# Performance work log

Measured on AMD Instinct MI355X. Metric: run time of the kernel, lower is better.

## Reference

```python
import jax, jax.numpy as jnp
from jax import lax
import numpy as np

B, TIN, F, H, TOUT = 256, 512, 64, 512, 64


def setup_inputs() -> dict:
    key = jax.random.key(0)
    ks = jax.random.split(key, 16)
    s = 0.05

    def p(k, shape):
        return jax.random.normal(k, shape, jnp.float32) * s

    inp = {
        "x": jax.random.normal(ks[0], (B, TIN, F), jnp.float32),
        "y": jax.random.normal(ks[1], (B, TOUT), jnp.float32),
    }
    i = 2
    for name, insz in [("enc0", F), ("enc1", H), ("dec0", 1), ("dec1", H)]:
        inp[name + "_Wih"] = p(ks[i], (4 * H, insz)); i += 1
        inp[name + "_Whh"] = p(ks[i], (4 * H, H)); i += 1
        inp[name + "_bih"] = jnp.zeros((4 * H,), jnp.float32)
        inp[name + "_bhh"] = jnp.zeros((4 * H,), jnp.float32)
    inp["proj_W"] = p(ks[i], (1, H)); i += 1
    inp["proj_b"] = jnp.zeros((1,), jnp.float32)
    return inp


def _cell(xt, h, c, Wih, Whh, bih, bhh):
    # PyTorch gate order: i, f, g, o
    g = xt @ Wih.T + h @ Whh.T + bih + bhh  # [B, 4H]
    i, f, gg, o = jnp.split(g, 4, axis=-1)
    c = jax.nn.sigmoid(f) * c + jax.nn.sigmoid(i) * jnp.tanh(gg)
    h = jax.nn.sigmoid(o) * jnp.tanh(c)
    return h, c


def reference(x, y,
              enc0_Wih, enc0_Whh, enc0_bih, enc0_bhh,
              enc1_Wih, enc1_Whh, enc1_bih, enc1_bhh,
              dec0_Wih, dec0_Whh, dec0_bih, dec0_bhh,
              dec1_Wih, dec1_Whh, dec1_bih, dec1_bhh,
              proj_W, proj_b):
    Bsz = x.shape[0]
    Hd = enc0_Whh.shape[1]
    Tout = y.shape[1]
    z = jnp.zeros((Bsz, Hd), x.dtype)

    def enc_step(carry, xt):
        h0, c0, h1, c1 = carry
        h0, c0 = _cell(xt, h0, c0, enc0_Wih, enc0_Whh, enc0_bih, enc0_bhh)
        h1, c1 = _cell(h0, h1, c1, enc1_Wih, enc1_Whh, enc1_bih, enc1_bhh)
        return (h0, c0, h1, c1), None

    (h0, c0, h1, c1), _ = lax.scan(enc_step, (z, z, z, z), jnp.swapaxes(x, 0, 1))

    prev = x[:, -1, -1:]  # [B, 1]

    def dec_step(carry, _):
        h0, c0, h1, c1, prev = carry
        h0, c0 = _cell(prev, h0, c0, dec0_Wih, dec0_Whh, dec0_bih, dec0_bhh)
        h1, c1 = _cell(h0, h1, c1, dec1_Wih, dec1_Whh, dec1_bih, dec1_bhh)
        step = h1 @ proj_W.T + proj_b  # [B, 1]
        # teacher_forcing = 0.0 -> always feed model prediction back
        return (h0, c0, h1, c1, step), step[:, 0]

    _, outs = lax.scan(dec_step, (h0, c0, h1, c1, prev), None, length=Tout)
    return outs.T  # [B, Tout]
```

## Files before the change

### kernel.cpp

```cpp
#include <hip/hip_runtime.h>

#define TINN 512
#define FF 64
#define HHD 512
#define TOUTN 64

using v8h = __attribute__((ext_vector_type(8))) _Float16;
using v4h = __attribute__((ext_vector_type(4))) _Float16;
using v4f = __attribute__((ext_vector_type(4))) float;
using u32x4 = __attribute__((ext_vector_type(4))) unsigned int;
using u64 = unsigned long long;

#define AGT __HIP_MEMORY_SCOPE_AGENT

#define WOFF 0
#define BIAS_OFF 131072
#define WIH0_OFF 131328
#define PREV_OFF 131584
#define PART_OFF 131840
#define PROJW_OFF 132864
#define PROJB_OFF 134912
#define TRANS_OFF 134976
#define SMEM_TOTAL 137024

#define WS_BAR 0
#define WS_HOFF 16384
#define HBYTES (256 * HHD * 2)
#define WS_XS (WS_HOFF + 6 * HBYTES)
#define XS_TBYTES 32768
#define WS_NEED (WS_XS + (size_t)TINN * XS_TBYTES)

static __device__ __forceinline__ float sigm(float x) { return 1.0f / (1.0f + __expf(-x)); }
static __device__ __forceinline__ float tanh_f(float x) { return 1.0f - 2.0f / (1.0f + __expf(2.0f * x)); }

static __device__ __forceinline__ v8h aload16(const _Float16* p) {
  union { u64 u[2]; v8h h; } c;
  const u64* q = (const u64*)p;
  c.u[0] = __hip_atomic_load(q, __ATOMIC_RELAXED, AGT);
  c.u[1] = __hip_atomic_load(q + 1, __ATOMIC_RELAXED, AGT);
  return c.h;
}
static __device__ __forceinline__ void astore8(_Float16* p, v4h v) {
  union { u64 u; v4h h; } c;
  c.h = v;
  __hip_atomic_store((u64*)p, c.u, __ATOMIC_RELAXED, AGT);
}
static __device__ __forceinline__ void astore8z(void* p) {
  __hip_atomic_store((u64*)p, 0ull, __ATOMIC_RELAXED, AGT);
}

#if __has_builtin(__builtin_amdgcn_raw_ptr_buffer_load_b128) && \
    __has_builtin(__builtin_amdgcn_make_buffer_rsrc)
#define HAVE_BUFLOAD 1
using rsrc_t = __amdgpu_buffer_rsrc_t;
static __device__ __forceinline__ rsrc_t mkrsrc(const void* p) {
  return __builtin_amdgcn_make_buffer_rsrc((void*)p, (short)0, 0xFFFFFFFFu, 0x00020000);
}
static __device__ __forceinline__ v8h bload16(rsrc_t r, int byteOff) {
  union { u32x4 u; v8h h; } c;
  c.u = __builtin_amdgcn_raw_ptr_buffer_load_b128(r, byteOff, 0, 17);
  return c.h;
}
#endif

static __device__ __forceinline__ void signalDone(unsigned* slots, int mySlot, unsigned val) {
  __builtin_amdgcn_s_waitcnt(0);
  __syncthreads();
  if (threadIdx.x == 0)
    __hip_atomic_store(&slots[(size_t)mySlot * 16], val, __ATOMIC_RELAXED, AGT);
}

static __device__ __forceinline__ void waitRole(unsigned* slots, int base, int tgt) {
  if (tgt > 0) {
    if (threadIdx.x < 32) {
      while ((int)__hip_atomic_load(&slots[(size_t)(base + threadIdx.x) * 16],
                                    __ATOMIC_RELAXED, AGT) < tgt)
        __builtin_amdgcn_s_sleep(1);
    }
    __syncthreads();
#if __has_builtin(__builtin_amdgcn_sched_barrier)
    __builtin_amdgcn_sched_barrier(0);
#endif
  }
}

static __device__ __forceinline__ void waitRoles(unsigned* slots, int tgt0, int tgt1) {
  int t = threadIdx.x;
  if (t < 64) {
    int tgt = (t < 32) ? tgt0 : tgt1;
    if (tgt > 0) {
      unsigned* p = &slots[(size_t)t * 16];
      while ((int)__hip_atomic_load(p, __ATOMIC_RELAXED, AGT) < tgt)
        __builtin_amdgcn_s_sleep(1);
    }
  }
  __syncthreads();
#if __has_builtin(__builtin_amdgcn_sched_barrier)
  __builtin_amdgcn_sched_barrier(0);
#endif
}

static __device__ __attribute__((noinline)) void loadWeights(
    int tid, int hc0, const float* W1, int ld1, int K1,
    const float* W2, int K) {
  extern __shared__ char smem[];
  int c = tid >> 2, sub = tid & 3;
  int nt = c >> 4, l = c & 15;
  int n = nt * HHD + hc0 + l;
  int Kq = K >> 2;
  for (int k = sub * Kq; k < (sub + 1) * Kq; ++k) {
    float v;
    if (k < K1) v = W1[(size_t)n * ld1 + k];
    else        v = W2[(size_t)n * HHD + (k - K1)];
    int kc = k >> 6, ks = (k >> 5) & 1, quad = (k >> 3) & 3, j = k & 7;
    int off = (((kc * 2 + ks) * 4 + nt) * 64 + quad * 16 + l) * 16 + j * 2;
    *(_Float16*)(smem + WOFF + off) = (_Float16)v;
  }
}

template <int WC0>
static __device__ __forceinline__ void mfma8(
    const _Float16* src, int rt, int lane, const char* wbLane, v4f* acc) {
#if HAVE_BUFLOAD
  rsrc_t rs = mkrsrc(src);
#endif
#pragma unroll
  for (int kc = 0; kc < 8; ++kc) {
    int off = rt * 16384 + kc * 2048 + lane * 16;
    v8h ak0, ak1;
#if HAVE_BUFLOAD
    ak0 = bload16(rs, off);
    ak1 = bload16(rs, off + 1024);
#else
    ak0 = aload16(src + off / 2);
    ak1 = aload16(src + (off + 1024) / 2);
#endif
    const char* bb = wbLane + (size_t)(WC0 + kc) * 8192;
#pragma unroll
    for (int ks = 0; ks < 2; ++ks) {
      v8h a = ks ? ak1 : ak0;
      acc[0] = __builtin_amdgcn_mfma_f32_16x16x32_f16(a, *(const v8h*)(bb + (ks * 4 + 0) * 1024), acc[0], 0, 0, 0);
      acc[1] = __builtin_amdgcn_mfma_f32_16x16x32_f16(a, *(const v8h*)(bb + (ks * 4 + 1) * 1024), acc[1], 0, 0, 0);
      acc[2] = __builtin_amdgcn_mfma_f32_16x16x32_f16(a, *(const v8h*)(bb + (ks * 4 + 2) * 1024), acc[2], 0, 0, 0);
      acc[3] = __builtin_amdgcn_mfma_f32_16x16x32_f16(a, *(const v8h*)(bb + (ks * 4 + 3) * 1024), acc[3], 0, 0, 0);
    }
  }
}

static __device__ __forceinline__ void mfmaDual(
    const _Float16* h0src, const _Float16* h1src, int rt, int lane,
    const char* wbLane, v4f* acc) {
  v8h a1[16], a0[16];
#if HAVE_BUFLOAD
  rsrc_t r1 = mkrsrc(h1src);
  rsrc_t r0 = mkrsrc(h0src);
#pragma unroll
  for (int kc = 0; kc < 8; ++kc) {
    int off = rt * 16384 + kc * 2048 + lane * 16;
    a1[2 * kc]     = bload16(r1, off);
    a1[2 * kc + 1] = bload16(r1, off + 1024);
  }
#pragma unroll
  for (int kc = 0; kc < 8; ++kc) {
    int off = rt * 16384 + kc * 2048 + lane * 16;
    a0[2 * kc]     = bload16(r0, off);
    a0[2 * kc + 1] = bload16(r0, off + 1024);
  }
#else
#pragma unroll
  for (int kc = 0; kc < 8; ++kc) {
    int off = rt * 16384 + kc * 2048 + lane * 16;
    a1[2 * kc]     = aload16(h1src + off / 2);
    a1[2 * kc + 1] = aload16(h1src + (off + 1024) / 2);
  }
#pragma unroll
  for (int kc = 0; kc < 8; ++kc) {
    int off = rt * 16384 + kc * 2048 + lane * 16;
    a0[2 * kc]     = aload16(h0src + off / 2);
    a0[2 * kc + 1] = aload16(h0src + (off + 1024) / 2);
  }
#endif
#pragma unroll
  for (int kc = 0; kc < 8; ++kc) {
    const char* bb = wbLane + (size_t)(8 + kc) * 8192;
#pragma unroll
    for (int ks = 0; ks < 2; ++ks) {
      v8h a = a1[2 * kc + ks];
      acc[0] = __builtin_amdgcn_mfma_f32_16x16x32_f16(a, *(const v8h*)(bb + (ks * 4 + 0) * 1024), acc[0], 0, 0, 0);
      acc[1] = __builtin_amdgcn_mfma_f32_16x16x32_f16(a, *(const v8h*)(bb + (ks * 4 + 1) * 1024), acc[1], 0, 0, 0);
      acc[2] = __builtin_amdgcn_mfma_f32_16x16x32_f16(a, *(const v8h*)(bb + (ks * 4 + 2) * 1024), acc[2], 0, 0, 0);
      acc[3] = __builtin_amdgcn_mfma_f32_16x16x32_f16(a, *(const v8h*)(bb + (ks * 4 + 3) * 1024), acc[3], 0, 0, 0);
    }
  }
#pragma unroll
  for (int kc = 0; kc < 8; ++kc) {
    const char* bb = wbLane + (size_t)kc * 8192;
#pragma unroll
    for (int ks = 0; ks < 2; ++ks) {
      v8h a = a0[2 * kc + ks];
      acc[0] = __builtin_amdgcn_mfma_f32_16x16x32_f16(a, *(const v8h*)(bb + (ks * 4 + 0) * 1024), acc[0], 0, 0, 0);
      acc[1] = __builtin_amdgcn_mfma_f32_16x16x32_f16(a, *(const v8h*)(bb + (ks * 4 + 1) * 1024), acc[1], 0, 0, 0);
      acc[2] = __builtin_amdgcn_mfma_f32_16x16x32_f16(a, *(const v8h*)(bb + (ks * 4 + 2) * 1024), acc[2], 0, 0, 0);
      acc[3] = __builtin_amdgcn_mfma_f32_16x16x32_f16(a, *(const v8h*)(bb + (ks * 4 + 3) * 1024), acc[3], 0, 0, 0);
    }
  }
}

static __device__ __forceinline__ void xChunk(
    const char* xsT, const float* xstep, int m0, int tid,
    const char* wbLane, v4f* acc) {
  int lane = tid & 63, wave = tid >> 6;
  int l15 = lane & 15, quad = lane >> 4;
  v8h ak0, ak1;
  if (xsT != nullptr) {
    int rt = (m0 >> 4) + wave;
    const char* xb = xsT + rt * 2048 + lane * 16;
    ak0 = *(const v8h*)(xb);
    ak1 = *(const v8h*)(xb + 1024);
  } else {
    int ra = m0 + wave * 16 + l15;
    const float* xr = xstep + (size_t)ra * (TINN * FF) + quad * 8;
    v4f f00 = *(const v4f*)(xr);
    v4f f01 = *(const v4f*)(xr + 4);
    v4f f10 = *(const v4f*)(xr + 32);
    v4f f11 = *(const v4f*)(xr + 36);
#pragma unroll
    for (int e = 0; e < 4; ++e) {
      ak0[e] = (_Float16)f00[e]; ak0[4 + e] = (_Float16)f01[e];
      ak1[e] = (_Float16)f10[e]; ak1[4 + e] = (_Float16)f11[e];
    }
  }
#pragma unroll
  for (int ks = 0; ks < 2; ++ks) {
    v8h a = ks ? ak1 : ak0;
    acc[0] = __builtin_amdgcn_mfma_f32_16x16x32_f16(a, *(const v8h*)(wbLane + (ks * 4 + 0) * 1024), acc[0], 0, 0, 0);
    acc[1] = __builtin_amdgcn_mfma_f32_16x16x32_f16(a, *(const v8h*)(wbLane + (ks * 4 + 1) * 1024), acc[1], 0, 0, 0);
    acc[2] = __builtin_amdgcn_mfma_f32_16x16x32_f16(a, *(const v8h*)(wbLane + (ks * 4 + 2) * 1024), acc[2], 0, 0, 0);
    acc[3] = __builtin_amdgcn_mfma_f32_16x16x32_f16(a, *(const v8h*)(wbLane + (ks * 4 + 3) * 1024), acc[3], 0, 0, 0);
  }
}

static __device__ __forceinline__ void epilogue(
    int tid, int m0, int hc0, int rank1, _Float16* hout, float* creg, v4f* acc) {
  extern __shared__ char smem[];
  int lane = tid & 63, wave = tid >> 6;
  int l15 = lane & 15, quad = lane >> 4;
  float* bias = (float*)(smem + BIAS_OFF);
  float bi = bias[l15], bf = bias[16 + l15], bg = bias[32 + l15], bo = bias[48 + l15];
  float wi = 0.f, wf = 0.f, wg = 0.f, wo = 0.f;
  if (rank1) {
    float* wih0 = (float*)(smem + WIH0_OFF);
    wi = wih0[l15]; wf = wih0[16 + l15]; wg = wih0[32 + l15]; wo = wih0[48 + l15];
  }
  float* prevl = (float*)(smem + PREV_OFF);
  _Float16* tb = (_Float16*)(smem + TRANS_OFF + (size_t)wave * 512);
#pragma unroll
  for (int r = 0; r < 4; ++r) {
    int mloc = wave * 16 + quad * 4 + r;
    float gi = acc[0][r] + bi, gf = acc[1][r] + bf;
    float gg = acc[2][r] + bg, go = acc[3][r] + bo;
    if (rank1) {
      float pv = prevl[mloc];
      gi += pv * wi; gf += pv * wf; gg += pv * wg; go += pv * wo;
    }
    float cc = sigm(gf) * creg[r] + sigm(gi) * tanh_f(gg);
    float h = sigm(go) * tanh_f(cc);
    creg[r] = cc;
    tb[(quad * 4 + r) * 16 + l15] = (_Float16)h;
  }
  {
    int mloc = lane & 15, cg = lane >> 4;
    v4h hv = *(const v4h*)(tb + mloc * 16 + cg * 4);
    int m = m0 + wave * 16 + mloc;
    int c0 = hc0 + cg * 4;
    int off = (m >> 4) * 16384 + (c0 >> 6) * 2048 + ((c0 >> 5) & 1) * 1024 +
              ((c0 >> 3) & 3) * 256 + (m & 15) * 16 + (c0 & 7) * 2;
    astore8((_Float16*)((char*)hout + off), hv);
  }
}


static __device__ __attribute__((noinline)) void stepEnc0(
    int tid, int m0, int hc0, unsigned* slots, int mySlot, int p,
    const char* xsT, const float* xstep,
    const _Float16* h0prev, _Float16* h0out, float* creg) {
  extern __shared__ char smem[];
  int lane = tid & 63, wave = tid >> 6;
  v4f acc[4];
  acc[0] = v4f{0.f, 0.f, 0.f, 0.f}; acc[1] = acc[0]; acc[2] = acc[0]; acc[3] = acc[0];
  const char* wbLane = smem + WOFF + (size_t)lane * 16;
  if (p == 0) {
    waitRoles(slots, 1, 0);
    xChunk(xsT, xstep, m0, tid, wbLane, acc);
  } else {
    xChunk(xsT, xstep, m0, tid, wbLane, acc);
    waitRoles(slots, p + 1, p - 2);
  }
  mfma8<1>(h0prev, (m0 >> 4) + wave, lane, wbLane, acc);
  epilogue(tid, m0, hc0, 0, h0out, creg, acc);
  signalDone(slots, mySlot, p + 2);
}

static __device__ __attribute__((noinline)) void stepL1(
    int tid, int m0, int hc0, unsigned* slots, int mySlot, int tR1, int tR0,
    const _Float16* h0src, const _Float16* h1prev, _Float16* h1out, float* creg) {
  extern __shared__ char smem[];
  int lane = tid & 63, wave = tid >> 6;
  v4f acc[4];
  acc[0] = v4f{0.f, 0.f, 0.f, 0.f}; acc[1] = acc[0]; acc[2] = acc[0]; acc[3] = acc[0];
  const char* wbLane = smem + WOFF + (size_t)lane * 16;
  int rt = (m0 >> 4) + wave;
  waitRoles(slots, tR0, tR1);
  mfmaDual(h0src, h1prev, rt, lane, wbLane, acc);
  epilogue(tid, m0, hc0, 0, h1out, creg, acc);
  signalDone(slots, mySlot, tR0);
}

static __device__ __attribute__((noinline)) void stepDec0(
    int tid, int m0, int hc0, unsigned* slots, int mySlot, int u,
    const _Float16* h0prev, _Float16* h0out, float* creg) {
  extern __shared__ char smem[];
  int lane = tid & 63, wave = tid >> 6;
  v4f acc[4];
  acc[0] = v4f{0.f, 0.f, 0.f, 0.f}; acc[1] = acc[0]; acc[2] = acc[0]; acc[3] = acc[0];
  const char* wbLane = smem + WOFF + (size_t)lane * 16;
  waitRole(slots, 0, u + 1);
  mfma8<0>(h0prev, (m0 >> 4) + wave, lane, wbLane, acc);
  epilogue(tid, m0, hc0, 1, h0out, creg, acc);
  signalDone(slots, mySlot, u + 2);
}

__global__ void __launch_bounds__(256, 1)
seq2seq_kernel(const float* x,
               const float* e0wi, const float* e0wh, const float* e0bi, const float* e0bh,
               const float* e1wi, const float* e1wh, const float* e1bi, const float* e1bh,
               const float* d0wi, const float* d0wh, const float* d0bi, const float* d0bh,
               const float* d1wi, const float* d1wh, const float* d1bi, const float* d1bh,
               const float* pw, const float* pb,
               float* out, char* ws, int useXs) {
  extern __shared__ char smem[];
  int tid = threadIdx.x, bid = blockIdx.x;
  int group = bid >> 6;
  int r = bid & 63;
  bool isL1 = (r >= 32);
  int hcTile = r & 31;
  int hc0 = hcTile * 16;
  int m0 = group * 64;
  unsigned* slots = (unsigned*)(ws + WS_BAR) + (size_t)group * 1024;
  int mySlot = isL1 ? 32 + hcTile : hcTile;
  char* xs = useXs ? (ws + WS_XS) : nullptr;

  _Float16* h0b[4]; _Float16* h1b[2];
  h0b[0] = (_Float16*)(ws + WS_HOFF);
  h0b[1] = (_Float16*)(ws + WS_HOFF + 1 * HBYTES);
  h0b[2] = (_Float16*)(ws + WS_HOFF + 2 * HBYTES);
  h0b[3] = (_Float16*)(ws + WS_HOFF + 3 * HBYTES);
  h1b[0] = (_Float16*)(ws + WS_HOFF + 4 * HBYTES);
  h1b[1] = (_Float16*)(ws + WS_HOFF + 5 * HBYTES);

  float creg[4];
  creg[0] = 0.f; creg[1] = 0.f; creg[2] = 0.f; creg[3] = 0.f;

  {
    int t16 = r * 256 + tid;
    char* base = (t16 < 8192) ? (char*)h0b[3] : (char*)h1b[1];
    int idx = t16 & 8191;
    astore8z(base + (size_t)m0 * HHD * 2 + (size_t)idx * 8);
  }

  if (xs) {
    int m = m0 + (tid & 63);
    int cb = (tid >> 6) * 16;
    int rt = m >> 4, l15m = m & 15;
    for (int k = 0; k < 8; ++k) {
      int t = r + k * 64;
      const float* xp = x + (size_t)m * (TINN * FF) + (size_t)t * FF + cb;
      v4f f0 = *(const v4f*)(xp);
      v4f f1 = *(const v4f*)(xp + 4);
      v4f f2 = *(const v4f*)(xp + 8);
      v4f f3 = *(const v4f*)(xp + 12);
      v4h h0_, h1_, h2_, h3_;
#pragma unroll
      for (int e = 0; e < 4; ++e) {
        h0_[e] = (_Float16)f0[e]; h1_[e] = (_Float16)f1[e];
        h2_[e] = (_Float16)f2[e]; h3_[e] = (_Float16)f3[e];
      }
      char* xt = xs + (size_t)t * XS_TBYTES;
      v4h hs[4] = {h0_, h1_, h2_, h3_};
#pragma unroll
      for (int s = 0; s < 4; ++s) {
        int c0 = cb + 4 * s;
        int off = (rt * 2 + ((c0 >> 5) & 1)) * 1024 +
                  ((c0 >> 3) & 3) * 256 + l15m * 16 + (c0 & 7) * 2;
        astore8((_Float16*)(xt + off), hs[s]);
      }
    }
  }

  if (!isL1) {
    loadWeights(tid, hc0, e0wi, 64, 64, e0wh, 576);
    if (tid < 64) {
      int n = (tid >> 4) * HHD + hc0 + (tid & 15);
      ((float*)(smem + BIAS_OFF))[tid] = e0bi[n] + e0bh[n];
    }
  } else {
    loadWeights(tid, hc0, e1wi, 512, 512, e1wh, 1024);
    if (tid < 64) {
      int n = (tid >> 4) * HHD + hc0 + (tid & 15);
      ((float*)(smem + BIAS_OFF))[tid] = e1bi[n] + e1bh[n];
    }
  }
  signalDone(slots, mySlot, 1);

  if (!isL1) {
    for (int p = 0; p < TINN; ++p)
      stepEnc0(tid, m0, hc0, slots, mySlot, p,
               xs ? xs + (size_t)p * XS_TBYTES : nullptr,
               xs ? nullptr : x + (size_t)p * FF,
               h0b[(p + 3) & 3], h0b[p & 3], creg);
    loadWeights(tid, hc0, d0wh, 512, 512, nullptr, 512);
    if (tid < 64) {
      int n = (tid >> 4) * HHD + hc0 + (tid & 15);
      ((float*)(smem + BIAS_OFF))[tid] = d0bi[n] + d0bh[n];
      ((float*)(smem + WIH0_OFF))[tid] = d0wi[n];
    }
    for (int k = tid; k < 512; k += 256) ((float*)(smem + PROJW_OFF))[k] = pw[k];
    if (tid == 0) ((float*)(smem + PROJB_OFF))[0] = pb[0];
    for (int t = 0; t <= TOUTN; ++t) {
      int u = TINN + t;
      waitRole(slots, 32, u + 1);
      float* prevl = (float*)(smem + PREV_OFF);
      if (t == 0) {
        if (tid < 64)
          prevl[tid] = x[(size_t)(m0 + tid) * (TINN * FF) + 511 * 64 + 63];
      } else {
        float* part = (float*)(smem + PART_OFF);
        float* pjw = (float*)(smem + PROJW_OFF);
        const _Float16* h1base = h1b[(u + 1) & 1];
        int m = m0 + (tid >> 2);
        int rt = m >> 4, l15m = m & 15;
        int kc0 = (tid & 3) * 2;
        float s = 0.f;
#pragma unroll
        for (int kc = kc0; kc < kc0 + 2; ++kc)
#pragma unroll
          for (int ks = 0; ks < 2; ++ks)
#pragma unroll
            for (int q = 0; q < 4; ++q) {
              int off = (rt * 8 + kc) * 2048 + ks * 1024 + q * 256 + l15m * 16;
              v8h hv = aload16(h1base + off / 2);
              const float* w = pjw + kc * 64 + ks * 32 + q * 8;
#pragma unroll
              for (int e = 0; e < 8; ++e) s += (float)hv[e] * w[e];
            }
        part[tid] = s;
        __syncthreads();
        if (tid < 64) {
          float p4 = part[tid * 4] + part[tid * 4 + 1] + part[tid * 4 + 2] +
                     part[tid * 4 + 3] + ((float*)(smem + PROJB_OFF))[0];
          prevl[tid] = p4;
          if (hcTile == 0) out[(size_t)(m0 + tid) * TOUTN + (t - 1)] = p4;
        }
      }
      __syncthreads();
      if (t < TOUTN)
        stepDec0(tid, m0, hc0, slots, mySlot, u, h0b[(u + 3) & 3], h0b[u & 3], creg);
    }
  } else {
    for (int s = 0; s < TINN; ++s)
      stepL1(tid, m0, hc0, slots, mySlot, s + 1, s + 2,
             h0b[s & 3], h1b[(s + 1) & 1], h1b[s & 1], creg);
    loadWeights(tid, hc0, d1wi, 512, 512, d1wh, 1024);
    if (tid < 64) {
      int n = (tid >> 4) * HHD + hc0 + (tid & 15);
      ((float*)(smem + BIAS_OFF))[tid] = d1bi[n] + d1bh[n];
    }
    for (int t = 0; t < TOUTN; ++t) {
      int u = TINN + t;
      stepL1(tid, m0, hc0, slots, mySlot, u + 1, u + 2,
             h0b[u & 3], h1b[(u + 1) & 1], h1b[u & 1], creg);
    }
  }
}

extern "C" void kernel_launch(void* const* d_in, const int* in_sizes, int n_in,
                              void* d_out, int out_size, void* d_ws, size_t ws_size,
                              hipStream_t stream) {
  const float* x = (const float*)d_in[0];
  const float* e0wi = (const float*)d_in[2];
  const float* e0wh = (const float*)d_in[3];
  const float* e0bi = (const float*)d_in[4];
  const float* e0bh = (const float*)d_in[5];
  const float* e1wi = (const float*)d_in[6];
  const float* e1wh = (const float*)d_in[7];
  const float* e1bi = (const float*)d_in[8];
  const float* e1bh = (const float*)d_in[9];
  const float* d0wi = (const float*)d_in[10];
  const float* d0wh = (const float*)d_in[11];
  const float* d0bi = (const float*)d_in[12];
  const float* d0bh = (const float*)d_in[13];
  const float* d1wi = (const float*)d_in[14];
  const float* d1wh = (const float*)d_in[15];
  const float* d1bi = (const float*)d_in[16];
  const float* d1bh = (const float*)d_in[17];
  const float* pw = (const float*)d_in[18];
  const float* pb = (const float*)d_in[19];

  int useXs = (ws_size >= WS_NEED) ? 1 : 0;
  (void)hipFuncSetAttribute((const void*)seq2seq_kernel,
                            hipFuncAttributeMaxDynamicSharedMemorySize, SMEM_TOTAL);
  (void)hipMemsetAsync(d_ws, 0, 16384, stream);
  seq2seq_kernel<<<dim3(256), dim3(256), SMEM_TOTAL, stream>>>(
      x, e0wi, e0wh, e0bi, e0bh, e1wi, e1wh, e1bi, e1bh,
      d0wi, d0wh, d0bi, d0bh, d1wi, d1wh, d1bi, d1bh,
      pw, pb, (float*)d_out, (char*)d_ws, useXs);
}
```

Before: 4.478 ms.

## Replicate completion flags per consumer block to avoid shared-slot polling contention

```diff
diff --git a/kernel.cpp b/kernel.cpp
--- a/kernel.cpp
+++ b/kernel.cpp
@@ -24,7 +24,8 @@
 #define SMEM_TOTAL 137024
 
 #define WS_BAR 0
-#define WS_HOFF 16384
+#define WS_FLAG_BYTES (4 * 64 * 64 * 64)
+#define WS_HOFF WS_FLAG_BYTES
 #define HBYTES (256 * HHD * 2)
 #define WS_XS (WS_HOFF + 6 * HBYTES)
 #define XS_TBYTES 32768
@@ -63,18 +64,20 @@
 }
 #endif
 
-static __device__ __forceinline__ void signalDone(unsigned* slots, int mySlot, unsigned val) {
+static __device__ __forceinline__ void signalDone(unsigned* flagsG, int mySlot, unsigned val) {
   __builtin_amdgcn_s_waitcnt(0);
   __syncthreads();
-  if (threadIdx.x == 0)
-    __hip_atomic_store(&slots[(size_t)mySlot * 16], val, __ATOMIC_RELAXED, AGT);
-}
-
-static __device__ __forceinline__ void waitRole(unsigned* slots, int base, int tgt) {
+  if (threadIdx.x < 64) {
+    unsigned* p = flagsG + ((size_t)threadIdx.x * 64 + mySlot) * 16;
+    __hip_atomic_store(p, val, __ATOMIC_RELAXED, AGT);
+  }
+}
+
+static __device__ __forceinline__ void waitRolePriv(unsigned* myflags, int base, int tgt) {
   if (tgt > 0) {
     if (threadIdx.x < 32) {
-      while ((int)__hip_atomic_load(&slots[(size_t)(base + threadIdx.x) * 16],
-                                    __ATOMIC_RELAXED, AGT) < tgt)
+      unsigned* p = myflags + (size_t)(base + threadIdx.x) * 16;
+      while ((int)__hip_atomic_load(p, __ATOMIC_RELAXED, AGT) < tgt)
         __builtin_amdgcn_s_sleep(1);
     }
     __syncthreads();
@@ -84,12 +87,12 @@
   }
 }
 
-static __device__ __forceinline__ void waitRoles(unsigned* slots, int tgt0, int tgt1) {
+static __device__ __forceinline__ void waitRolesPriv(unsigned* myflags, int tgt0, int tgt1) {
   int t = threadIdx.x;
   if (t < 64) {
     int tgt = (t < 32) ? tgt0 : tgt1;
     if (tgt > 0) {
-      unsigned* p = &slots[(size_t)t * 16];
+      unsigned* p = myflags + (size_t)t * 16;
       while ((int)__hip_atomic_load(p, __ATOMIC_RELAXED, AGT) < tgt)
         __builtin_amdgcn_s_sleep(1);
     }
@@ -281,7 +284,7 @@
 
 
 static __device__ __attribute__((noinline)) void stepEnc0(
-    int tid, int m0, int hc0, unsigned* slots, int mySlot, int p,
+    int tid, int m0, int hc0, unsigned* flagsG, unsigned* myflags, int mySlot, int p,
     const char* xsT, const float* xstep,
     const _Float16* h0prev, _Float16* h0out, float* creg) {
   extern __shared__ char smem[];
@@ -290,19 +293,20 @@
   acc[0] = v4f{0.f, 0.f, 0.f, 0.f}; acc[1] = acc[0]; acc[2] = acc[0]; acc[3] = acc[0];
   const char* wbLane = smem + WOFF + (size_t)lane * 16;
   if (p == 0) {
-    waitRoles(slots, 1, 0);
+    waitRolesPriv(myflags, 1, 0);
     xChunk(xsT, xstep, m0, tid, wbLane, acc);
   } else {
     xChunk(xsT, xstep, m0, tid, wbLane, acc);
-    waitRoles(slots, p + 1, p - 2);
+    waitRolesPriv(myflags, p + 1, p - 2);
   }
   mfma8<1>(h0prev, (m0 >> 4) + wave, lane, wbLane, acc);
   epilogue(tid, m0, hc0, 0, h0out, creg, acc);
-  signalDone(slots, mySlot, p + 2);
+  signalDone(flagsG, mySlot, p + 2);
 }
 
 static __device__ __attribute__((noinline)) void stepL1(
-    int tid, int m0, int hc0, unsigned* slots, int mySlot, int tR1, int tR0,
+    int tid, int m0, int hc0, unsigned* flagsG, unsigned* myflags, int mySlot,
+    int tR1, int tR0,
     const _Float16* h0src, const _Float16* h1prev, _Float16* h1out, float* creg) {
   extern __shared__ char smem[];
   int lane = tid & 63, wave = tid >> 6;
@@ -310,24 +314,24 @@
   acc[0] = v4f{0.f, 0.f, 0.f, 0.f}; acc[1] = acc[0]; acc[2] = acc[0]; acc[3] = acc[0];
   const char* wbLane = smem + WOFF + (size_t)lane * 16;
   int rt = (m0 >> 4) + wave;
-  waitRoles(slots, tR0, tR1);
+  waitRolesPriv(myflags, tR0, tR1);
   mfmaDual(h0src, h1prev, rt, lane, wbLane, acc);
   epilogue(tid, m0, hc0, 0, h1out, creg, acc);
-  signalDone(slots, mySlot, tR0);
+  signalDone(flagsG, mySlot, tR0);
 }
 
 static __device__ __attribute__((noinline)) void stepDec0(
-    int tid, int m0, int hc0, unsigned* slots, int mySlot, int u,
+    int tid, int m0, int hc0, unsigned* flagsG, unsigned* myflags, int mySlot, int u,
     const _Float16* h0prev, _Float16* h0out, float* creg) {
   extern __shared__ char smem[];
   int lane = tid & 63, wave = tid >> 6;
   v4f acc[4];
   acc[0] = v4f{0.f, 0.f, 0.f, 0.f}; acc[1] = acc[0]; acc[2] = acc[0]; acc[3] = acc[0];
   const char* wbLane = smem + WOFF + (size_t)lane * 16;
-  waitRole(slots, 0, u + 1);
+  waitRolePriv(myflags, 0, u + 1);
   mfma8<0>(h0prev, (m0 >> 4) + wave, lane, wbLane, acc);
   epilogue(tid, m0, hc0, 1, h0out, creg, acc);
-  signalDone(slots, mySlot, u + 2);
+  signalDone(flagsG, mySlot, u + 2);
 }
 
 __global__ void __launch_bounds__(256, 1)
@@ -346,7 +350,8 @@
   int hcTile = r & 31;
   int hc0 = hcTile * 16;
   int m0 = group * 64;
-  unsigned* slots = (unsigned*)(ws + WS_BAR) + (size_t)group * 1024;
+  unsigned* flagsG = (unsigned*)(ws + WS_BAR) + (size_t)group * 64 * 64 * 16;
+  unsigned* myflags = flagsG + (size_t)r * 64 * 16;
   int mySlot = isL1 ? 32 + hcTile : hcTile;
   char* xs = useXs ? (ws + WS_XS) : nullptr;
 
@@ -410,11 +415,11 @@
       ((float*)(smem + BIAS_OFF))[tid] = e1bi[n] + e1bh[n];
     }
   }
-  signalDone(slots, mySlot, 1);
+  signalDone(flagsG, mySlot, 1);
 
   if (!isL1) {
     for (int p = 0; p < TINN; ++p)
-      stepEnc0(tid, m0, hc0, slots, mySlot, p,
+      stepEnc0(tid, m0, hc0, flagsG, myflags, mySlot, p,
                xs ? xs + (size_t)p * XS_TBYTES : nullptr,
                xs ? nullptr : x + (size_t)p * FF,
                h0b[(p + 3) & 3], h0b[p & 3], creg);
@@ -428,7 +433,7 @@
     if (tid == 0) ((float*)(smem + PROJB_OFF))[0] = pb[0];
     for (int t = 0; t <= TOUTN; ++t) {
       int u = TINN + t;
-      waitRole(slots, 32, u + 1);
+      waitRolePriv(myflags, 32, u + 1);
       float* prevl = (float*)(smem + PREV_OFF);
       if (t == 0) {
         if (tid < 64)
@@ -464,11 +469,12 @@
       }
       __syncthreads();
       if (t < TOUTN)
-        stepDec0(tid, m0, hc0, slots, mySlot, u, h0b[(u + 3) & 3], h0b[u & 3], creg);
+        stepDec0(tid, m0, hc0, flagsG, myflags, mySlot, u,
+                 h0b[(u + 3) & 3], h0b[u & 3], creg);
     }
   } else {
     for (int s = 0; s < TINN; ++s)
-      stepL1(tid, m0, hc0, slots, mySlot, s + 1, s + 2,
+      stepL1(tid, m0, hc0, flagsG, myflags, mySlot, s + 1, s + 2,
              h0b[s & 3], h1b[(s + 1) & 1], h1b[s & 1], creg);
     loadWeights(tid, hc0, d1wi, 512, 512, d1wh, 1024);
     if (tid < 64) {
@@ -477,7 +483,7 @@
     }
     for (int t = 0; t < TOUTN; ++t) {
       int u = TINN + t;
-      stepL1(tid, m0, hc0, slots, mySlot, u + 1, u + 2,
+      stepL1(tid, m0, hc0, flagsG, myflags, mySlot, u + 1, u + 2,
              h0b[u & 3], h1b[(u + 1) & 1], h1b[u & 1], creg);
     }
   }
@@ -509,7 +515,7 @@
   int useXs = (ws_size >= WS_NEED) ? 1 : 0;
   (void)hipFuncSetAttribute((const void*)seq2seq_kernel,
                             hipFuncAttributeMaxDynamicSharedMemorySize, SMEM_TOTAL);
-  (void)hipMemsetAsync(d_ws, 0, 16384, stream);
+  (void)hipMemsetAsync(d_ws, 0, WS_FLAG_BYTES, stream);
   seq2seq_kernel<<<dim3(256), dim3(256), SMEM_TOTAL, stream>>>(
       x, e0wi, e0wh, e0bi, e0bh, e1wi, e1wh, e1bi, e1bh,
       d0wi, d0wh, d0bi, d0bh, d1wi, d1wh, d1bi, d1bh,
```

After: 4.453 ms. About the same (-0.5%).

## Replace per-block flag slots with shared atomic counters and drop x pre-staging

Applied to the files above, without the earlier changes.

```diff
diff --git a/kernel.cpp b/kernel.cpp
--- a/kernel.cpp
+++ b/kernel.cpp
@@ -23,15 +23,18 @@
 #define TRANS_OFF 134976
 #define SMEM_TOTAL 137024
 
-#define WS_BAR 0
+#define WS_CNT 0
 #define WS_HOFF 16384
 #define HBYTES (256 * HHD * 2)
-#define WS_XS (WS_HOFF + 6 * HBYTES)
-#define XS_TBYTES 32768
-#define WS_NEED (WS_XS + (size_t)TINN * XS_TBYTES)
 
 static __device__ __forceinline__ float sigm(float x) { return 1.0f / (1.0f + __expf(-x)); }
 static __device__ __forceinline__ float tanh_f(float x) { return 1.0f - 2.0f / (1.0f + __expf(2.0f * x)); }
+
+static __device__ __forceinline__ void schedBar() {
+#if __has_builtin(__builtin_amdgcn_sched_barrier)
+  __builtin_amdgcn_sched_barrier(0);
+#endif
+}
 
 static __device__ __forceinline__ v8h aload16(const _Float16* p) {
   union { u64 u[2]; v8h h; } c;
@@ -63,41 +66,30 @@
 }
 #endif
 
-static __device__ __forceinline__ void signalDone(unsigned* slots, int mySlot, unsigned val) {
+static __device__ __forceinline__ void signalDone(unsigned* cntMine) {
   __builtin_amdgcn_s_waitcnt(0);
   __syncthreads();
   if (threadIdx.x == 0)
-    __hip_atomic_store(&slots[(size_t)mySlot * 16], val, __ATOMIC_RELAXED, AGT);
-}
-
-static __device__ __forceinline__ void waitRole(unsigned* slots, int base, int tgt) {
-  if (tgt > 0) {
-    if (threadIdx.x < 32) {
-      while ((int)__hip_atomic_load(&slots[(size_t)(base + threadIdx.x) * 16],
-                                    __ATOMIC_RELAXED, AGT) < tgt)
-        __builtin_amdgcn_s_sleep(1);
-    }
-    __syncthreads();
-#if __has_builtin(__builtin_amdgcn_sched_barrier)
-    __builtin_amdgcn_sched_barrier(0);
-#endif
-  }
-}
-
-static __device__ __forceinline__ void waitRoles(unsigned* slots, int tgt0, int tgt1) {
+    (void)__hip_atomic_fetch_add(cntMine, 1u, __ATOMIC_RELAXED, AGT);
+}
+
+static __device__ __forceinline__ void spinCnt(unsigned* p, int tgt) {
+  unsigned goal = (unsigned)(32 * tgt);
+  for (;;) {
+    unsigned v = __hip_atomic_load(p, __ATOMIC_RELAXED, AGT);
+    if (v >= goal) break;
+    asm volatile("" ::: "memory");
+    __builtin_amdgcn_s_sleep(2);
+  }
+}
+
+static __device__ __forceinline__ void waitCnts(
+    unsigned* cnt0, unsigned* cnt1, int tgt0, int tgt1) {
   int t = threadIdx.x;
-  if (t < 64) {
-    int tgt = (t < 32) ? tgt0 : tgt1;
-    if (tgt > 0) {
-      unsigned* p = &slots[(size_t)t * 16];
-      while ((int)__hip_atomic_load(p, __ATOMIC_RELAXED, AGT) < tgt)
-        __builtin_amdgcn_s_sleep(1);
-    }
-  }
+  if (t == 0 && tgt0 > 0) spinCnt(cnt0, tgt0);
+  if (t == 1 && tgt1 > 0) spinCnt(cnt1, tgt1);
   __syncthreads();
-#if __has_builtin(__builtin_amdgcn_sched_barrier)
-  __builtin_amdgcn_sched_barrier(0);
-#endif
+  schedBar();
 }
 
 static __device__ __attribute__((noinline)) void loadWeights(
@@ -207,28 +199,20 @@
 }
 
 static __device__ __forceinline__ void xChunk(
-    const char* xsT, const float* xstep, int m0, int tid,
-    const char* wbLane, v4f* acc) {
+    const float* xstep, int m0, int tid, const char* wbLane, v4f* acc) {
   int lane = tid & 63, wave = tid >> 6;
   int l15 = lane & 15, quad = lane >> 4;
   v8h ak0, ak1;
-  if (xsT != nullptr) {
-    int rt = (m0 >> 4) + wave;
-    const char* xb = xsT + rt * 2048 + lane * 16;
-    ak0 = *(const v8h*)(xb);
-    ak1 = *(const v8h*)(xb + 1024);
-  } else {
-    int ra = m0 + wave * 16 + l15;
-    const float* xr = xstep + (size_t)ra * (TINN * FF) + quad * 8;
-    v4f f00 = *(const v4f*)(xr);
-    v4f f01 = *(const v4f*)(xr + 4);
-    v4f f10 = *(const v4f*)(xr + 32);
-    v4f f11 = *(const v4f*)(xr + 36);
-#pragma unroll
-    for (int e = 0; e < 4; ++e) {
-      ak0[e] = (_Float16)f00[e]; ak0[4 + e] = (_Float16)f01[e];
-      ak1[e] = (_Float16)f10[e]; ak1[4 + e] = (_Float16)f11[e];
-    }
+  int ra = m0 + wave * 16 + l15;
+  const float* xr = xstep + (size_t)ra * (TINN * FF) + quad * 8;
+  v4f f00 = *(const v4f*)(xr);
+  v4f f01 = *(const v4f*)(xr + 4);
+  v4f f10 = *(const v4f*)(xr + 32);
+  v4f f11 = *(const v4f*)(xr + 36);
+#pragma unroll
+  for (int e = 0; e < 4; ++e) {
+    ak0[e] = (_Float16)f00[e]; ak0[4 + e] = (_Float16)f01[e];
+    ak1[e] = (_Float16)f10[e]; ak1[4 + e] = (_Float16)f11[e];
   }
 #pragma unroll
   for (int ks = 0; ks < 2; ++ks) {
@@ -281,28 +265,22 @@
 
 
 static __device__ __attribute__((noinline)) void stepEnc0(
-    int tid, int m0, int hc0, unsigned* slots, int mySlot, int p,
-    const char* xsT, const float* xstep,
-    const _Float16* h0prev, _Float16* h0out, float* creg) {
+    int tid, int m0, int hc0, unsigned* cnt0, unsigned* cnt1, int p,
+    const float* xstep, const _Float16* h0prev, _Float16* h0out, float* creg) {
   extern __shared__ char smem[];
   int lane = tid & 63, wave = tid >> 6;
   v4f acc[4];
   acc[0] = v4f{0.f, 0.f, 0.f, 0.f}; acc[1] = acc[0]; acc[2] = acc[0]; acc[3] = acc[0];
   const char* wbLane = smem + WOFF + (size_t)lane * 16;
-  if (p == 0) {
-    waitRoles(slots, 1, 0);
-    xChunk(xsT, xstep, m0, tid, wbLane, acc);
-  } else {
-    xChunk(xsT, xstep, m0, tid, wbLane, acc);
-    waitRoles(slots, p + 1, p - 2);
-  }
+  xChunk(xstep, m0, tid, wbLane, acc);
+  waitCnts(cnt0, cnt1, p + 1, p - 2);
   mfma8<1>(h0prev, (m0 >> 4) + wave, lane, wbLane, acc);
   epilogue(tid, m0, hc0, 0, h0out, creg, acc);
-  signalDone(slots, mySlot, p + 2);
+  signalDone(cnt0);
 }
 
 static __device__ __attribute__((noinline)) void stepL1(
-    int tid, int m0, int hc0, unsigned* slots, int mySlot, int tR1, int tR0,
+    int tid, int m0, int hc0, unsigned* cnt0, unsigned* cnt1, int tR1, int tR0,
     const _Float16* h0src, const _Float16* h1prev, _Float16* h1out, float* creg) {
   extern __shared__ char smem[];
   int lane = tid & 63, wave = tid >> 6;
@@ -310,24 +288,24 @@
   acc[0] = v4f{0.f, 0.f, 0.f, 0.f}; acc[1] = acc[0]; acc[2] = acc[0]; acc[3] = acc[0];
   const char* wbLane = smem + WOFF + (size_t)lane * 16;
   int rt = (m0 >> 4) + wave;
-  waitRoles(slots, tR0, tR1);
+  waitCnts(cnt0, cnt1, tR0, tR1);
   mfmaDual(h0src, h1prev, rt, lane, wbLane, acc);
   epilogue(tid, m0, hc0, 0, h1out, creg, acc);
-  signalDone(slots, mySlot, tR0);
+  signalDone(cnt1);
 }
 
 static __device__ __attribute__((noinline)) void stepDec0(
-    int tid, int m0, int hc0, unsigned* slots, int mySlot, int u,
+    int tid, int m0, int hc0, unsigned* cnt0, unsigned* cnt1, int u,
     const _Float16* h0prev, _Float16* h0out, float* creg) {
   extern __shared__ char smem[];
   int lane = tid & 63, wave = tid >> 6;
   v4f acc[4];
   acc[0] = v4f{0.f, 0.f, 0.f, 0.f}; acc[1] = acc[0]; acc[2] = acc[0]; acc[3] = acc[0];
   const char* wbLane = smem + WOFF + (size_t)lane * 16;
-  waitRole(slots, 0, u + 1);
+  waitCnts(cnt0, cnt1, u + 1, 0);
   mfma8<0>(h0prev, (m0 >> 4) + wave, lane, wbLane, acc);
   epilogue(tid, m0, hc0, 1, h0out, creg, acc);
-  signalDone(slots, mySlot, u + 2);
+  signalDone(cnt0);
 }
 
 __global__ void __launch_bounds__(256, 1)
@@ -337,7 +315,7 @@
                const float* d0wi, const float* d0wh, const float* d0bi, const float* d0bh,
                const float* d1wi, const float* d1wh, const float* d1bi, const float* d1bh,
                const float* pw, const float* pb,
-               float* out, char* ws, int useXs) {
+               float* out, char* ws) {
   extern __shared__ char smem[];
   int tid = threadIdx.x, bid = blockIdx.x;
   int group = bid >> 6;
@@ -346,9 +324,8 @@
   int hcTile = r & 31;
   int hc0 = hcTile * 16;
   int m0 = group * 64;
-  unsigned* slots = (unsigned*)(ws + WS_BAR) + (size_t)group * 1024;
-  int mySlot = isL1 ? 32 + hcTile : hcTile;
-  char* xs = useXs ? (ws + WS_XS) : nullptr;
+  unsigned* cnt0 = (unsigned*)(ws + WS_CNT) + (size_t)group * 32;
+  unsigned* cnt1 = cnt0 + 16;
 
   _Float16* h0b[4]; _Float16* h1b[2];
   h0b[0] = (_Float16*)(ws + WS_HOFF);
@@ -368,35 +345,6 @@
     astore8z(base + (size_t)m0 * HHD * 2 + (size_t)idx * 8);
   }
 
-  if (xs) {
-    int m = m0 + (tid & 63);
-    int cb = (tid >> 6) * 16;
-    int rt = m >> 4, l15m = m & 15;
-    for (int k = 0; k < 8; ++k) {
-      int t = r + k * 64;
-      const float* xp = x + (size_t)m * (TINN * FF) + (size_t)t * FF + cb;
-      v4f f0 = *(const v4f*)(xp);
-      v4f f1 = *(const v4f*)(xp + 4);
-      v4f f2 = *(const v4f*)(xp + 8);
-      v4f f3 = *(const v4f*)(xp + 12);
-      v4h h0_, h1_, h2_, h3_;
-#pragma unroll
-      for (int e = 0; e < 4; ++e) {
-        h0_[e] = (_Float16)f0[e]; h1_[e] = (_Float16)f1[e];
-        h2_[e] = (_Float16)f2[e]; h3_[e] = (_Float16)f3[e];
-      }
-      char* xt = xs + (size_t)t * XS_TBYTES;
-      v4h hs[4] = {h0_, h1_, h2_, h3_};
-#pragma unroll
-      for (int s = 0; s < 4; ++s) {
-        int c0 = cb + 4 * s;
-        int off = (rt * 2 + ((c0 >> 5) & 1)) * 1024 +
-                  ((c0 >> 3) & 3) * 256 + l15m * 16 + (c0 & 7) * 2;
-        astore8((_Float16*)(xt + off), hs[s]);
-      }
-    }
-  }
-
   if (!isL1) {
     loadWeights(tid, hc0, e0wi, 64, 64, e0wh, 576);
     if (tid < 64) {
@@ -410,13 +358,11 @@
       ((float*)(smem + BIAS_OFF))[tid] = e1bi[n] + e1bh[n];
     }
   }
-  signalDone(slots, mySlot, 1);
+  signalDone(isL1 ? cnt1 : cnt0);
 
   if (!isL1) {
     for (int p = 0; p < TINN; ++p)
-      stepEnc0(tid, m0, hc0, slots, mySlot, p,
-               xs ? xs + (size_t)p * XS_TBYTES : nullptr,
-               xs ? nullptr : x + (size_t)p * FF,
+      stepEnc0(tid, m0, hc0, cnt0, cnt1, p, x + (size_t)p * FF,
                h0b[(p + 3) & 3], h0b[p & 3], creg);
     loadWeights(tid, hc0, d0wh, 512, 512, nullptr, 512);
     if (tid < 64) {
@@ -426,9 +372,10 @@
     }
     for (int k = tid; k < 512; k += 256) ((float*)(smem + PROJW_OFF))[k] = pw[k];
     if (tid == 0) ((float*)(smem + PROJB_OFF))[0] = pb[0];
+    __syncthreads();
     for (int t = 0; t <= TOUTN; ++t) {
       int u = TINN + t;
-      waitRole(slots, 32, u + 1);
+      waitCnts(cnt0, cnt1, 0, u + 1);
       float* prevl = (float*)(smem + PREV_OFF);
       if (t == 0) {
         if (tid < 64)
@@ -464,11 +411,11 @@
       }
       __syncthreads();
       if (t < TOUTN)
-        stepDec0(tid, m0, hc0, slots, mySlot, u, h0b[(u + 3) & 3], h0b[u & 3], creg);
+        stepDec0(tid, m0, hc0, cnt0, cnt1, u, h0b[(u + 3) & 3], h0b[u & 3], creg);
     }
   } else {
     for (int s = 0; s < TINN; ++s)
-      stepL1(tid, m0, hc0, slots, mySlot, s + 1, s + 2,
+      stepL1(tid, m0, hc0, cnt0, cnt1, s + 1, s + 2,
              h0b[s & 3], h1b[(s + 1) & 1], h1b[s & 1], creg);
     loadWeights(tid, hc0, d1wi, 512, 512, d1wh, 1024);
     if (tid < 64) {
@@ -477,7 +424,7 @@
     }
     for (int t = 0; t < TOUTN; ++t) {
       int u = TINN + t;
-      stepL1(tid, m0, hc0, slots, mySlot, u + 1, u + 2,
+      stepL1(tid, m0, hc0, cnt0, cnt1, u + 1, u + 2,
              h0b[u & 3], h1b[(u + 1) & 1], h1b[u & 1], creg);
     }
   }
@@ -506,12 +453,11 @@
   const float* pw = (const float*)d_in[18];
   const float* pb = (const float*)d_in[19];
 
-  int useXs = (ws_size >= WS_NEED) ? 1 : 0;
   (void)hipFuncSetAttribute((const void*)seq2seq_kernel,
                             hipFuncAttributeMaxDynamicSharedMemorySize, SMEM_TOTAL);
   (void)hipMemsetAsync(d_ws, 0, 16384, stream);
   seq2seq_kernel<<<dim3(256), dim3(256), SMEM_TOTAL, stream>>>(
       x, e0wi, e0wh, e0bi, e0bh, e1wi, e1wh, e1bi, e1bh,
       d0wi, d0wh, d0bi, d0bh, d1wi, d1wh, d1bi, d1bh,
-      pw, pb, (float*)d_out, (char*)d_ws, useXs);
-}
+      pw, pb, (float*)d_out, (char*)d_ws);
+}
```

Result: slower. 4.973 ms (+11.1%).
